# Kernel tuning notes

Measured on AMD Instinct MI355X. Metric: run time of the kernel, lower is better.

Reference implementation:

```python
import math
import jax, jax.numpy as jnp
import numpy as np

T, C, NH = 2048, 1024, 16
HD = C // NH


def setup_inputs() -> dict:
    key = jax.random.key(0)
    ks = jax.random.split(key, 5)
    return {
        "x": jax.random.normal(ks[0], (T, C), dtype=jnp.float32),
        "w_attn": jax.random.normal(ks[1], (3 * C, C), dtype=jnp.float32) * (1.0 / math.sqrt(C)),
        "b_attn": jax.random.normal(ks[2], (3 * C,), dtype=jnp.float32) * 0.02,
        "w_proj": jax.random.normal(ks[3], (C, C), dtype=jnp.float32) * (1.0 / math.sqrt(C)),
        "b_proj": jax.random.normal(ks[4], (C,), dtype=jnp.float32) * 0.02,
    }


def reference(x, w_attn, b_attn, w_proj, b_proj):
    t, c = x.shape
    # qkv projection: eqx Linear computes W @ x + b, vmapped over T
    qkv = x @ w_attn.T + b_attn  # (T, 3C)
    q, k, v = jnp.split(qkv, 3, axis=1)  # each (T, C)
    # (T, NH, HD) -> (NH, T, HD)
    q = jnp.swapaxes(q.reshape(t, NH, HD), 0, 1)
    k = jnp.swapaxes(k.reshape(t, NH, HD), 0, 1)
    v = jnp.swapaxes(v.reshape(t, NH, HD), 0, 1)
    att = jnp.einsum('hqd,hkd->hqk', q, k) / math.sqrt(HD)  # (NH, T, T)
    causal = jnp.tril(jnp.ones((t, t), dtype=bool))
    att = jnp.where(causal[None, :, :], att, -jnp.inf)
    att = jax.nn.softmax(att, axis=-1)
    y = jnp.matmul(att, v)  # (NH, T, HD)
    # Faithful to source: swapaxes(1,2) on (NH, T, HD) -> (NH, HD, T), then reshape
    y = jnp.swapaxes(y, 1, 2).reshape(t, c)
    return y @ w_proj.T + b_proj
```

## Files before the change

kernel.cpp:

```cpp
#include <hip/hip_runtime.h>
#include <hip/hip_bf16.h>
#include <stdint.h>

typedef __bf16 bf16;
typedef __bf16 bf16x8 __attribute__((ext_vector_type(8)));
typedef __bf16 bf16x4 __attribute__((ext_vector_type(4)));
typedef float floatx4 __attribute__((ext_vector_type(4)));
typedef short short4v __attribute__((ext_vector_type(4)));

#define T_DIM 2048
#define C_DIM 1024
#define NH    16
#define HD    64

__device__ __forceinline__ void gload_lds16(const void* g, void* l) {
    __builtin_amdgcn_global_load_lds(
        (__attribute__((address_space(1))) void*)(g),
        (__attribute__((address_space(3))) void*)(l),
        16, 0, 0);
}

#define MFMA16(a, b, c)  __builtin_amdgcn_mfma_f32_16x16x32_bf16(a, b, c, 0, 0, 0)
#define MFMAK16(a, b, c) __builtin_amdgcn_mfma_f32_16x16x16bf16_1k(a, b, c, 0, 0, 0)

__global__ __launch_bounds__(256) void cvt_all(
    const float* __restrict__ x, const float* __restrict__ wa,
    const float* __restrict__ wp,
    bf16* __restrict__ xb, bf16* __restrict__ wab, bf16* __restrict__ wpb)
{
    const int i = blockIdx.x * 256 + threadIdx.x;
    const float* src; bf16* dst; int off;
    if (i < 262144)      { src = x;  dst = xb;  off = i; }
    else if (i < 655360) { src = wa; dst = wab; off = i - 262144; }
    else                 { src = wp; dst = wpb; off = i - 655360; }
    const float4 a = ((const float4*)src)[off * 2];
    const float4 b = ((const float4*)src)[off * 2 + 1];
    bf16x8 o;
    o[0] = (bf16)a.x; o[1] = (bf16)a.y; o[2] = (bf16)a.z; o[3] = (bf16)a.w;
    o[4] = (bf16)b.x; o[5] = (bf16)b.y; o[6] = (bf16)b.z; o[7] = (bf16)b.w;
    *(bf16x8*)(dst + (size_t)off * 8) = o;
}

template<int MODE, int TN>
__global__ __launch_bounds__(256) void csa_gemm_bt(
    const bf16* __restrict__ A, const bf16* __restrict__ B,
    const float* __restrict__ bias,
    void* __restrict__ out0v, bf16* __restrict__ out1, bf16* __restrict__ out2)
{
    constexpr int K = 1024;
    constexpr int MT = (TN == 128) ? 4 : 2;
    __shared__ __align__(16) bf16 sA[128 * 32];
    __shared__ __align__(16) bf16 sB[TN * 32];

    const int tid  = threadIdx.x;
    const int lane = tid & 63;
    const int wid  = tid >> 6;
    const int rowbase = (TN == 128) ? (wid & 1) * 64 : wid * 32;
    const int colbase = (TN == 128) ? (wid >> 1) * 64 : 0;
    const int tileM = blockIdx.x * 128;
    const int tileN = blockIdx.y * TN;

    const int r0 = tid >> 2;
    const int c0 = (tid & 3) * 8;
    const long aBase = (long)(tileM + r0) * K + c0;
    const long bBase = (long)(tileN + r0) * K + c0;

    const int fr   = lane & 15;
    const int quad = lane >> 4;
    const int fc   = quad * 8;

    floatx4 acc[MT][4];
#pragma unroll
    for (int i = 0; i < MT; i++)
#pragma unroll
        for (int j = 0; j < 4; j++) acc[i][j] = (floatx4){0.f, 0.f, 0.f, 0.f};

    for (int k0 = 0; k0 < K; k0 += 32) {
        __syncthreads();
        gload_lds16(A + aBase + k0,                 sA + tid * 8);
        gload_lds16(A + aBase + (long)64 * K + k0,  sA + 2048 + tid * 8);
        gload_lds16(B + bBase + k0,                 sB + tid * 8);
        if (TN == 128)
            gload_lds16(B + bBase + (long)64 * K + k0, sB + 2048 + tid * 8);
        __syncthreads();

        bf16x8 af[MT], bfr[4];
#pragma unroll
        for (int mt = 0; mt < MT; mt++)
            af[mt] = *(const bf16x8*)(sA + (rowbase + mt * 16 + fr) * 32 + fc);
#pragma unroll
        for (int nt = 0; nt < 4; nt++)
            bfr[nt] = *(const bf16x8*)(sB + (colbase + nt * 16 + fr) * 32 + fc);
#pragma unroll
        for (int mt = 0; mt < MT; mt++)
#pragma unroll
            for (int nt = 0; nt < 4; nt++)
                acc[mt][nt] = MFMA16(af[mt], bfr[nt], acc[mt][nt]);
    }

#pragma unroll
    for (int mt = 0; mt < MT; mt++) {
#pragma unroll
        for (int nt = 0; nt < 4; nt++) {
            const int gn = tileN + colbase + nt * 16 + fr;
            const float bv = bias[gn];
            const int gmb = tileM + rowbase + mt * 16 + quad * 4;
            if (MODE == 0) {
                const int which = gn >> 10;
                const int w2 = gn & 1023;
                const int hh = w2 >> 6, d = w2 & 63;
                if (which == 2) {
                    bf16x4 pk;
#pragma unroll
                    for (int r = 0; r < 4; r++) pk[r] = (bf16)(acc[mt][nt][r] + bv);
                    *(bf16x4*)(out2 + ((long)(hh * HD + d) << 11) + gmb) = pk;
                } else {
                    bf16* dst = (which == 0) ? (bf16*)out0v : out1;
#pragma unroll
                    for (int r = 0; r < 4; r++)
                        dst[((long)hh * T_DIM + gmb + r) * HD + d] =
                            (bf16)(acc[mt][nt][r] + bv);
                }
            } else {
#pragma unroll
                for (int r = 0; r < 4; r++)
                    ((float*)out0v)[(long)(gmb + r) * C_DIM + gn] =
                        acc[mt][nt][r] + bv;
            }
        }
    }
}

__global__ __launch_bounds__(256) void csa_attn_chunk(
    const bf16* __restrict__ Qh, const bf16* __restrict__ Kh,
    const bf16* __restrict__ Vth, float* __restrict__ Opart,
    float* __restrict__ lpart, bf16* __restrict__ YY)
{
    __shared__ __align__(16) bf16 sK[2][64 * 64];
    __shared__ __align__(16) bf16 sV[2][64 * 64];

    const int c  = blockIdx.x;
    const int h  = blockIdx.y;
    const int qt = 31 - (int)blockIdx.z;
    const int nk = qt + 1;
    const int kt0 = c * 8;
    if (kt0 >= nk) return;
    const int ktend = (kt0 + 8 < nk) ? kt0 + 8 : nk;

    const int tid  = threadIdx.x;
    const int lane = tid & 63;
    const int wid  = tid >> 6;
    const int fr   = lane & 15;
    const int quad = lane >> 4;
    const int f7   = fr & 7;
    const int q0   = qt * 64;
    const int qg   = q0 + wid * 16 + fr;

    const bf16* qrow = Qh + ((long)h * T_DIM + qg) * HD;
    const bf16x8 qf0 = *(const bf16x8*)(qrow + quad * 8);
    const bf16x8 qf1 = *(const bf16x8*)(qrow + quad * 8 + 32);

    const int rb   = tid >> 3;
    const int cswz = (tid & 7) ^ (rb & 7);

    auto stage = [&](int b, int k0) {
        gload_lds16(Kh + ((long)(h * T_DIM + k0 + rb) << 6) + cswz * 8,
                    &sK[b][0] + tid * 8);
        gload_lds16(Kh + ((long)(h * T_DIM + k0 + rb + 32) << 6) + cswz * 8,
                    &sK[b][0] + 2048 + tid * 8);
        gload_lds16(Vth + ((long)(h * HD + rb) << 11) + k0 + cswz * 8,
                    &sV[b][0] + tid * 8);
        gload_lds16(Vth + ((long)(h * HD + rb + 32) << 11) + k0 + cswz * 8,
                    &sV[b][0] + 2048 + tid * 8);
    };

    stage(0, kt0 * 64);

    float l_i = 0.f;
    floatx4 o_acc[4];
#pragma unroll
    for (int d4 = 0; d4 < 4; d4++) o_acc[d4] = (floatx4){0.f, 0.f, 0.f, 0.f};

    for (int kt = kt0; kt < ktend; ++kt) {
        const int it = kt - kt0;
        __syncthreads();
        if (kt + 1 < ktend) stage((it + 1) & 1, (kt + 1) * 64);
        const bf16* K_ = &sK[it & 1][0];
        const bf16* V_ = &sV[it & 1][0];
        const int k0 = kt * 64;
        const bool diag = (kt == qt);

        short4v pa[4];
        float s = 0.f;
#pragma unroll
        for (int nt = 0; nt < 4; nt++) {
            const bf16* kr = K_ + (nt * 16 + fr) * 64;
            const bf16x8 ka0 = *(const bf16x8*)(kr + (quad ^ f7) * 8);
            const bf16x8 ka1 = *(const bf16x8*)(kr + ((quad + 4) ^ f7) * 8);
            floatx4 z = (floatx4){0.f, 0.f, 0.f, 0.f};
            z = MFMA16(ka0, qf0, z);
            z = MFMA16(ka1, qf1, z);
            const int kgb = k0 + nt * 16 + quad * 4;
            bf16x4 pk;
#pragma unroll
            for (int r = 0; r < 4; r++) {
                const float e = __builtin_amdgcn_exp2f(z[r] * 0.1803368801f);
                const float pv = (!diag || (kgb + r <= qg)) ? e : 0.f;
                s += pv;
                pk[r] = (bf16)pv;
            }
            pa[nt] = __builtin_bit_cast(short4v, pk);
        }
        s += __shfl_xor(s, 16);
        s += __shfl_xor(s, 32);
        l_i += s;

#pragma unroll
        for (int d4 = 0; d4 < 4; d4++) {
            const bf16* vrow = V_ + (d4 * 16 + fr) * 64;
#pragma unroll
            for (int nt = 0; nt < 4; nt++) {
                const short4v vb = __builtin_bit_cast(short4v,
                    *(const bf16x4*)(vrow +
                        (((2 * nt + (quad >> 1)) ^ f7) * 8) + (quad & 1) * 4));
                o_acc[d4] = MFMAK16(pa[nt], vb, o_acc[d4]);
            }
        }
    }

    if (kt0 == 0 && ktend == nk) {
        const float inv_self = 1.f / l_i;
        float inv[4];
#pragma unroll
        for (int r = 0; r < 4; r++) inv[r] = __shfl(inv_self, quad * 4 + r);
#pragma unroll
        for (int r = 0; r < 4; r++) {
            const int q = q0 + wid * 16 + quad * 4 + r;
            const int rq = q >> 10, cq = q & 1023;
#pragma unroll
            for (int d4 = 0; d4 < 4; d4++) {
                const int d = d4 * 16 + fr;
                YY[(long)(h * 128 + 2 * d + rq) * 1024 + cq] =
                    (bf16)(o_acc[d4][r] * inv[r]);
            }
        }
    } else {
        const long obase = ((long)((h * 32 + qt) * 4 + c)) * 4096;
#pragma unroll
        for (int d4 = 0; d4 < 4; d4++)
#pragma unroll
            for (int r = 0; r < 4; r++)
                Opart[obase + (wid * 16 + quad * 4 + r) * 64 + d4 * 16 + fr] =
                    o_acc[d4][r];
        if (quad == 0)
            lpart[((h * 32 + qt) * 4 + c) * 64 + wid * 16 + fr] = l_i;
    }
}

__global__ __launch_bounds__(256) void csa_combine(
    const float* __restrict__ Opart, const float* __restrict__ lpart,
    bf16* __restrict__ YY)
{
    const int qt = blockIdx.x + 8;
    const int h  = blockIdx.y;
    const int nc = (qt >> 3) + 1;
    const int t  = threadIdx.x;
    const int q  = t >> 2;
    const int d0 = (t & 3) * 16;

    const long obase = ((long)((h * 32 + qt) * 4)) * 4096 + q * 64 + d0;
    const int  lbase = (h * 32 + qt) * 4 * 64 + q;

    float4 acc[4] = {};
    float lq = 0.f;
    for (int c = 0; c < nc; c++) {
        const float4* src = (const float4*)(Opart + obase + (long)c * 4096);
#pragma unroll
        for (int j = 0; j < 4; j++) {
            const float4 v = src[j];
            acc[j].x += v.x; acc[j].y += v.y; acc[j].z += v.z; acc[j].w += v.w;
        }
        lq += lpart[lbase + c * 64];
    }
    const float inv = 1.f / lq;
    const int qglob = qt * 64 + q;
    const int rq = qglob >> 10, cq = qglob & 1023;
#pragma unroll
    for (int j = 0; j < 4; j++) {
        const float vv[4] = {acc[j].x, acc[j].y, acc[j].z, acc[j].w};
#pragma unroll
        for (int k = 0; k < 4; k++) {
            const int d = d0 + j * 4 + k;
            YY[(long)(h * 128 + 2 * d + rq) * 1024 + cq] = (bf16)(vv[k] * inv);
        }
    }
}

extern "C" void kernel_launch(void* const* d_in, const int* in_sizes, int n_in,
                              void* d_out, int out_size, void* d_ws, size_t ws_size,
                              hipStream_t stream) {
    (void)in_sizes; (void)n_in; (void)out_size; (void)ws_size;
    const float* x      = (const float*)d_in[0];
    const float* w_attn = (const float*)d_in[1];
    const float* b_attn = (const float*)d_in[2];
    const float* w_proj = (const float*)d_in[3];
    const float* b_proj = (const float*)d_in[4];

    bf16* xb  = (bf16*)d_ws;
    bf16* wab = xb  + (size_t)T_DIM * C_DIM;
    bf16* wpb = wab + (size_t)3 * C_DIM * C_DIM;
    bf16* Q   = wpb + (size_t)C_DIM * C_DIM;
    bf16* Kp  = Q   + (size_t)NH * T_DIM * HD;
    bf16* Vt  = Kp  + (size_t)NH * T_DIM * HD;
    bf16* YY  = Vt  + (size_t)NH * T_DIM * HD;
    float* Opart = (float*)(YY + (size_t)T_DIM * C_DIM);
    float* lpart = Opart + (size_t)16 * 32 * 4 * 4096;

    cvt_all<<<3072, 256, 0, stream>>>(x, w_attn, w_proj, xb, wab, wpb);

    csa_gemm_bt<0, 64><<<dim3(16, 48), 256, 0, stream>>>(xb, wab, b_attn, Q, Kp, Vt);
    csa_attn_chunk<<<dim3(4, NH, 32), 256, 0, stream>>>(Q, Kp, Vt, Opart, lpart, YY);
    csa_combine<<<dim3(24, NH), 256, 0, stream>>>(Opart, lpart, YY);
    csa_gemm_bt<1, 64><<<dim3(16, 16), 256, 0, stream>>>(YY, wpb, b_proj, d_out, nullptr, nullptr);
}
```

Measured before the change: 155.3 us.

## Double-buffer GEMM LDS tiles with BK=64, XOR swizzle, and smaller proj tiles

Restructures the bf16 GEMM to use double-buffered LDS stages with a K-step of 64, so global-to-LDS loads for the next tile are issued before the current tile is computed, removing one barrier per iteration. It adds an XOR swizzle on the 16-byte chunk index to avoid LDS bank conflicts on fragment reads. It also templates the M tile so the output projection runs with 64x64 tiles across twice as many blocks. LDS use per block rises, which may lower occupancy.

```diff
diff --git a/kernel.cpp b/kernel.cpp
--- a/kernel.cpp
+++ b/kernel.cpp
@@ -41,67 +41,97 @@
     *(bf16x8*)(dst + (size_t)off * 8) = o;
 }
 
-template<int MODE, int TN>
+template<int MODE, int TM, int TN>
 __global__ __launch_bounds__(256) void csa_gemm_bt(
     const bf16* __restrict__ A, const bf16* __restrict__ B,
     const float* __restrict__ bias,
     void* __restrict__ out0v, bf16* __restrict__ out1, bf16* __restrict__ out2)
 {
-    constexpr int K = 1024;
-    constexpr int MT = (TN == 128) ? 4 : 2;
-    __shared__ __align__(16) bf16 sA[128 * 32];
-    __shared__ __align__(16) bf16 sB[TN * 32];
+    constexpr int K   = 1024;
+    constexpr int WM  = (TM == 128) ? 4 : 2;
+    constexpr int WN  = 4 / WM;
+    constexpr int MT  = 2;
+    constexpr int NT  = TN / (16 * WN);
+    constexpr int ACH = TM / 32;
+    constexpr int BCH = TN / 32;
+    __shared__ __align__(16) bf16 sA[2][TM * 64];
+    __shared__ __align__(16) bf16 sB[2][TN * 64];
 
     const int tid  = threadIdx.x;
     const int lane = tid & 63;
     const int wid  = tid >> 6;
-    const int rowbase = (TN == 128) ? (wid & 1) * 64 : wid * 32;
-    const int colbase = (TN == 128) ? (wid >> 1) * 64 : 0;
-    const int tileM = blockIdx.x * 128;
+    const int wm   = wid & (WM - 1);
+    const int wn   = wid / WM;
+    const int rowbase = wm * 32;
+    const int colbase = wn * (TN / WN);
+    const int tileM = blockIdx.x * TM;
     const int tileN = blockIdx.y * TN;
-
-    const int r0 = tid >> 2;
-    const int c0 = (tid & 3) * 8;
-    const long aBase = (long)(tileM + r0) * K + c0;
-    const long bBase = (long)(tileN + r0) * K + c0;
 
     const int fr   = lane & 15;
     const int quad = lane >> 4;
-    const int fc   = quad * 8;
-
-    floatx4 acc[MT][4];
+    const int f7   = fr & 7;
+
+    auto stage = [&](int b, int k0) {
+#pragma unroll
+        for (int i = 0; i < ACH; i++) {
+            const int cid = tid + 256 * i;
+            const int row = cid >> 3, pc = cid & 7;
+            gload_lds16(A + (long)(tileM + row) * K + k0 + (pc ^ (row & 7)) * 8,
+                        &sA[b][0] + cid * 8);
+        }
+#pragma unroll
+        for (int i = 0; i < BCH; i++) {
+            const int cid = tid + 256 * i;
+            const int row = cid >> 3, pc = cid & 7;
+            gload_lds16(B + (long)(tileN + row) * K + k0 + (pc ^ (row & 7)) * 8,
+                        &sB[b][0] + cid * 8);
+        }
+    };
+
+    floatx4 acc[MT][NT];
 #pragma unroll
     for (int i = 0; i < MT; i++)
 #pragma unroll
-        for (int j = 0; j < 4; j++) acc[i][j] = (floatx4){0.f, 0.f, 0.f, 0.f};
-
-    for (int k0 = 0; k0 < K; k0 += 32) {
+        for (int j = 0; j < NT; j++) acc[i][j] = (floatx4){0.f, 0.f, 0.f, 0.f};
+
+    stage(0, 0);
+
+    for (int it = 0; it < K / 64; ++it) {
         __syncthreads();
-        gload_lds16(A + aBase + k0,                 sA + tid * 8);
-        gload_lds16(A + aBase + (long)64 * K + k0,  sA + 2048 + tid * 8);
-        gload_lds16(B + bBase + k0,                 sB + tid * 8);
-        if (TN == 128)
-            gload_lds16(B + bBase + (long)64 * K + k0, sB + 2048 + tid * 8);
-        __syncthreads();
-
-        bf16x8 af[MT], bfr[4];
+        if (it + 1 < K / 64) stage((it + 1) & 1, (it + 1) * 64);
+        const bf16* A_ = &sA[it & 1][0];
+        const bf16* B_ = &sB[it & 1][0];
+
+        bf16x8 af[MT][2], bfr[NT][2];
+#pragma unroll
+        for (int mt = 0; mt < MT; mt++) {
+            const int row = rowbase + mt * 16 + fr;
+#pragma unroll
+            for (int kh = 0; kh < 2; kh++)
+                af[mt][kh] = *(const bf16x8*)(A_ + row * 64 +
+                                              ((kh * 4 + quad) ^ f7) * 8);
+        }
+#pragma unroll
+        for (int nt = 0; nt < NT; nt++) {
+            const int row = colbase + nt * 16 + fr;
+#pragma unroll
+            for (int kh = 0; kh < 2; kh++)
+                bfr[nt][kh] = *(const bf16x8*)(B_ + row * 64 +
+                                               ((kh * 4 + quad) ^ f7) * 8);
+        }
 #pragma unroll
         for (int mt = 0; mt < MT; mt++)
-            af[mt] = *(const bf16x8*)(sA + (rowbase + mt * 16 + fr) * 32 + fc);
-#pragma unroll
-        for (int nt = 0; nt < 4; nt++)
-            bfr[nt] = *(const bf16x8*)(sB + (colbase + nt * 16 + fr) * 32 + fc);
-#pragma unroll
-        for (int mt = 0; mt < MT; mt++)
-#pragma unroll
-            for (int nt = 0; nt < 4; nt++)
-                acc[mt][nt] = MFMA16(af[mt], bfr[nt], acc[mt][nt]);
+#pragma unroll
+            for (int nt = 0; nt < NT; nt++) {
+                acc[mt][nt] = MFMA16(af[mt][0], bfr[nt][0], acc[mt][nt]);
+                acc[mt][nt] = MFMA16(af[mt][1], bfr[nt][1], acc[mt][nt]);
+            }
     }
 
 #pragma unroll
     for (int mt = 0; mt < MT; mt++) {
 #pragma unroll
-        for (int nt = 0; nt < 4; nt++) {
+        for (int nt = 0; nt < NT; nt++) {
             const int gn = tileN + colbase + nt * 16 + fr;
             const float bv = bias[gn];
             const int gmb = tileM + rowbase + mt * 16 + quad * 4;
@@ -318,8 +348,8 @@
 
     cvt_all<<<3072, 256, 0, stream>>>(x, w_attn, w_proj, xb, wab, wpb);
 
-    csa_gemm_bt<0, 64><<<dim3(16, 48), 256, 0, stream>>>(xb, wab, b_attn, Q, Kp, Vt);
+    csa_gemm_bt<0, 128, 64><<<dim3(16, 48), 256, 0, stream>>>(xb, wab, b_attn, Q, Kp, Vt);
     csa_attn_chunk<<<dim3(4, NH, 32), 256, 0, stream>>>(Q, Kp, Vt, Opart, lpart, YY);
     csa_combine<<<dim3(24, NH), 256, 0, stream>>>(Opart, lpart, YY);
-    csa_gemm_bt<1, 64><<<dim3(16, 16), 256, 0, stream>>>(YY, wpb, b_proj, d_out, nullptr, nullptr);
-}
+    csa_gemm_bt<1, 64, 64><<<dim3(32, 16), 256, 0, stream>>>(YY, wpb, b_proj, d_out, nullptr, nullptr);
+}
```

Result: no change. 153.8 us (-1.0%).
